# Optimization experiments

Measured on AMD Instinct MI355X. Metric: run time of the kernel, lower is better.

Reference implementation:

```python
import jax, jax.numpy as jnp
import numpy as np

B = 1; S = 2048; HID = 1024; NH = 8; HD = 128; INTER = 4096
EPS = 1e-6; THETA = 10000.0


def rms_norm(x, w):
    # Gemma RMSNorm: x * rsqrt(mean(x^2)+eps) * (1 + w)
    v = jnp.mean(x * x, axis=-1, keepdims=True)
    return x * jax.lax.rsqrt(v + EPS) * (1.0 + w)


def rope_cos_sin(seqlen):
    inv = 1.0 / (THETA ** (jnp.arange(0, HD, 2, dtype=jnp.float32) / HD))
    t = jnp.arange(seqlen, dtype=jnp.float32)
    f = jnp.outer(t, inv)                       # (S, HD/2)
    emb = jnp.concatenate([f, f], axis=-1)      # (S, HD)
    return jnp.cos(emb), jnp.sin(emb)


def rotate_half(x):
    x1, x2 = jnp.split(x, 2, axis=-1)
    return jnp.concatenate([-x2, x1], axis=-1)


def apply_rope(x, cos, sin):
    return x * cos[None, None] + rotate_half(x) * sin[None, None]


def expert_forward(x, mask, params):
    """One GemmaDecoderLayer; returns output plus PRE-RoPE q/k/v (as the torch module exposes)."""
    w_ln, wq, wk, wv, wo, w_pln, wg, wu, wd = params
    res = x
    h = rms_norm(x, w_ln)

    def proj(w):
        return (h @ w).reshape(B, -1, NH, HD).transpose(0, 2, 1, 3)  # (B,H,S,D)

    q, k, v = proj(wq), proj(wk), proj(wv)      # stored before rotary in the original
    cos, sin = rope_cos_sin(x.shape[1])
    qr, kr = apply_rope(q, cos, sin), apply_rope(k, cos, sin)
    scores = jnp.einsum('bhqd,bhkd->bhqk', qr, kr) * (HD ** -0.5) + mask
    attn = jnp.einsum('bhqk,bhkd->bhqd', jax.nn.softmax(scores, axis=-1), v)
    attn = attn.transpose(0, 2, 1, 3).reshape(B, -1, NH * HD) @ wo
    h1 = res + attn
    m = rms_norm(h1, w_pln)
    mlp = (jax.nn.gelu(m @ wg, approximate=True) * (m @ wu)) @ wd  # gelu_pytorch_tanh
    return h1 + mlp, q, k, v


def setup_inputs() -> dict:
    key = jax.random.key(0)
    ks = iter(jax.random.split(key, 40))

    def w(shape, scale=0.02):
        return jax.random.normal(next(ks), shape, jnp.float32) * scale

    inp = {
        'x_a': jax.random.normal(next(ks), (B, S, HID), jnp.float32),
        'x_b': jax.random.normal(next(ks), (B, S, HID), jnp.float32),
    }
    tri = jnp.tril(jnp.ones((S, S), bool))
    causal = jnp.where(tri, 0.0, -1e9).astype(jnp.float32)[None, None]  # additive causal mask
    inp['mask_a'] = causal
    inp['mask_b'] = causal
    inp['mix_mask'] = jnp.zeros((B, 1, 2 * S, 2 * S), jnp.float32)      # non-causal cross-expert
    for e in ('a', 'b'):
        inp['w_ln_' + e] = jnp.zeros((HID,), jnp.float32)
        inp['w_q_' + e] = w((HID, NH * HD))
        inp['w_k_' + e] = w((HID, NH * HD))
        inp['w_v_' + e] = w((HID, NH * HD))
        inp['w_o_' + e] = w((NH * HD, HID))
        inp['w_pln_' + e] = jnp.zeros((HID,), jnp.float32)
        inp['w_g_' + e] = w((HID, INTER))
        inp['w_u_' + e] = w((HID, INTER))
        inp['w_d_' + e] = w((INTER, HID))
    return inp


def reference(x_a, x_b, mask_a, mask_b, mix_mask,
              w_ln_a, w_q_a, w_k_a, w_v_a, w_o_a, w_pln_a, w_g_a, w_u_a, w_d_a,
              w_ln_b, w_q_b, w_k_b, w_v_b, w_o_b, w_pln_b, w_g_b, w_u_b, w_d_b):
    pa = (w_ln_a, w_q_a, w_k_a, w_v_a, w_o_a, w_pln_a, w_g_a, w_u_a, w_d_a)
    pb = (w_ln_b, w_q_b, w_k_b, w_v_b, w_o_b, w_pln_b, w_g_b, w_u_b, w_d_b)
    out_a, qa, ka, va = expert_forward(x_a, mask_a, pa)
    out_b, qb, kb, vb = expert_forward(x_b, mask_b, pb)
    # cross-expert mixed attention over concatenated (pre-RoPE) streams
    q = jnp.concatenate([qa, qb], axis=2)
    k = jnp.concatenate([ka, kb], axis=2)
    v = jnp.concatenate([va, vb], axis=2)
    scores = jnp.einsum('bhqd,bhkd->bhqk', q, k) * (HD ** -0.5) + mix_mask
    mixed = jnp.einsum('bhqk,bhkd->bhqd', jax.nn.softmax(scores, axis=-1), v)
    mixed = mixed.transpose(0, 2, 1, 3).reshape(B, 2 * S, NH * HD)
    ma, mb = mixed[:, :S], mixed[:, S:]
    return jnp.stack([out_a + ma @ w_o_a, out_b + mb @ w_o_b])
```

## Files before the change

### kernel.cpp

```cpp
#include <hip/hip_runtime.h>
#include <hip/hip_bf16.h>
#include <math.h>

#define S 2048
#define HID 1024
#define NH 8
#define HD 128
#define INTER 4096
#define EPSV 1e-6f
#define THETA 10000.0f

typedef __hip_bfloat16 bf16;
typedef unsigned short u16;
typedef __attribute__((ext_vector_type(8))) short bf16x8;
typedef __attribute__((ext_vector_type(4))) float f32x4;

__device__ inline float bu2f(u16 u) {
    unsigned int x = ((unsigned int)u) << 16;
    return __uint_as_float(x);
}
__device__ inline u16 f2bu(float f) {
    bf16 h = __float2bfloat16(f);
    return *reinterpret_cast<u16*>(&h);
}
__device__ inline float ldin(const void* p, size_t i, bool isbf) {
    return isbf ? bu2f(((const u16*)p)[i]) : ((const float*)p)[i];
}
__device__ inline float gelu_tanh(float x) {
    float x3 = x * x * x;
    return 0.5f * x * (1.f + tanhf(0.7978845608028654f * (x + 0.044715f * x3)));
}
__device__ inline void gload16(const u16* g, u16* l) {
    __builtin_amdgcn_global_load_lds(
        (const __attribute__((address_space(1))) void*)g,
        (__attribute__((address_space(3))) void*)l, 16, 0, 0);
}

__global__ __launch_bounds__(256) void probe_kernel(const unsigned short* __restrict__ x,
                                                    int* __restrict__ flag) {
    __shared__ int red[256];
    int tid = threadIdx.x;
    int cnt = 0;
    for (int i = tid; i < 2048; i += 256) {
        unsigned short u = x[2 * i];
        int e = (u >> 7) & 0xFF;
        cnt += (e >= 110 && e <= 135) ? 1 : 0;
    }
    red[tid] = cnt;
    __syncthreads();
    for (int off = 128; off > 0; off >>= 1) {
        if (tid < off) red[tid] += red[tid + off];
        __syncthreads();
    }
    if (tid == 0) *flag = (red[0] > 1024) ? 1 : 0;
}

struct TransN {
    const void* W[8];
    u16* T[8];
};
__global__ __launch_bounds__(256) void transpose_wN(TransN tn, const int* __restrict__ flag,
                                                    int K, int N) {
    bool isbf = (*flag != 0);
    const void* W = tn.W[blockIdx.z];
    u16* WT = tn.T[blockIdx.z];
    __shared__ float t[32][33];
    int n0 = blockIdx.x * 32, k0 = blockIdx.y * 32;
    int c = threadIdx.x & 31, r = threadIdx.x >> 5;
#pragma unroll
    for (int p = 0; p < 4; p++)
        t[r + 8 * p][c] = ldin(W, (size_t)(k0 + r + 8 * p) * N + n0 + c, isbf);
    __syncthreads();
#pragma unroll
    for (int p = 0; p < 4; p++) {
        int row = r + 8 * p;
        WT[(size_t)(n0 + row) * K + k0 + c] = f2bu(t[c][row]);
    }
}

__global__ __launch_bounds__(256) void transpose_v(const u16* __restrict__ V0,
                                                   const u16* __restrict__ V1, int sv,
                                                   u16* __restrict__ VT) {
    const u16* V = blockIdx.z ? V1 : V0;
    VT += (size_t)blockIdx.z * ((size_t)NH * HD * S);
    __shared__ u16 t[32][33];
    int k0 = blockIdx.x * 32;
    int d0 = blockIdx.y * 32;
    int c = threadIdx.x & 31, r = threadIdx.x >> 5;
#pragma unroll
    for (int p = 0; p < 4; p++)
        t[r + 8 * p][c] = V[(size_t)(k0 + r + 8 * p) * sv + d0 + c];
    __syncthreads();
#pragma unroll
    for (int p = 0; p < 4; p++)
        VT[(size_t)(d0 + r + 8 * p) * S + k0 + c] = t[c][r + 8 * p];
}

struct RmsDual {
    const void* x[2];
    const void* w[2];
    u16* y[2];
};
__global__ __launch_bounds__(256) void rmsnorm_kernel(RmsDual rd,
                                                      const int* __restrict__ flag,
                                                      int dual) {
    int e = blockIdx.y;
    const void* x = rd.x[e];
    const void* w = rd.w[e];
    u16* y = rd.y[e];
    bool isbf = (*flag != 0);
    bool xbf = dual && isbf;
    int row = blockIdx.x;
    size_t base = (size_t)row * HID;
    __shared__ float red[256];
    float xv[4];
    float s = 0.f;
#pragma unroll
    for (int i = 0; i < 4; i++) {
        float v = ldin(x, base + threadIdx.x + 256 * i, xbf);
        xv[i] = v;
        s += v * v;
    }
    red[threadIdx.x] = s;
    __syncthreads();
    for (int off = 128; off > 0; off >>= 1) {
        if (threadIdx.x < off) red[threadIdx.x] += red[threadIdx.x + off];
        __syncthreads();
    }
    float scale = rsqrtf(red[0] / (float)HID + EPSV);
#pragma unroll
    for (int i = 0; i < 4; i++) {
        int c = threadIdx.x + 256 * i;
        y[base + c] = f2bu(xv[i] * scale * (1.f + ldin(w, c, isbf)));
    }
}

struct GemmDual {
    const u16* A[2];
    const u16* BT[2];
    float* Cf[2];
    u16* Cb[2];
    const void* res[2];
};
template <int BM, int BN, int WRN, int WCN, int EPI>
__global__ __launch_bounds__(256) void gemm_mfma(GemmDual g, const int* __restrict__ flag,
                                                 int M, int N, int K) {
    int eZ = blockIdx.z;
    const u16* __restrict__ A = g.A[eZ];
    const u16* __restrict__ BT = g.BT[eZ];
    float* __restrict__ Cf = g.Cf[eZ];
    u16* __restrict__ Cb = g.Cb[eZ];
    const void* __restrict__ res = g.res[eZ];
    constexpr int WM = BM / WRN, WN = BN / WCN, TI = WM / 16, TJ = WN / 16;
    __shared__ u16 As[2][BM * 32];
    __shared__ u16 Bs[2][BN * 32];
    int tid = threadIdx.x, lane = tid & 63, wv = tid >> 6;
    int wr = wv / WCN, wc = wv % WCN;
    int m = lane & 15, quad = lane >> 4;
    int m0 = blockIdx.y * BM, n0 = blockIdx.x * BN;
    f32x4 acc[TI][TJ] = {};
    for (int k0 = 0; k0 < K; k0 += 64) {
        __syncthreads();
#pragma unroll
        for (int pan = 0; pan < 2; pan++) {
            int kp = k0 + 32 * pan;
#pragma unroll
            for (int c2 = 0; c2 < BM / 64; c2++) {
                int row0 = (wv * (BM / 64) + c2) * 16;
                int row = row0 + (lane >> 2);
                int ch = lane & 3;
                gload16(&A[(size_t)(m0 + row) * K + kp + ((ch ^ ((row >> 1) & 3)) << 3)],
                        &As[pan][row0 * 32]);
            }
#pragma unroll
            for (int c2 = 0; c2 < BN / 64; c2++) {
                int row0 = (wv * (BN / 64) + c2) * 16;
                int row = row0 + (lane >> 2);
                int ch = lane & 3;
                gload16(&BT[(size_t)(n0 + row) * K + kp + ((ch ^ ((row >> 1) & 3)) << 3)],
                        &Bs[pan][row0 * 32]);
            }
        }
        __syncthreads();
#pragma unroll
        for (int pan = 0; pan < 2; pan++) {
            bf16x8 af[TI], bf_[TJ];
#pragma unroll
            for (int i = 0; i < TI; i++) {
                int rr = wr * WM + i * 16 + m;
                af[i] = *reinterpret_cast<const bf16x8*>(
                    &As[pan][rr * 32 + ((quad ^ ((rr >> 1) & 3)) << 3)]);
            }
#pragma unroll
            for (int j = 0; j < TJ; j++) {
                int rr = wc * WN + j * 16 + m;
                bf_[j] = *reinterpret_cast<const bf16x8*>(
                    &Bs[pan][rr * 32 + ((quad ^ ((rr >> 1) & 3)) << 3)]);
            }
#pragma unroll
            for (int i = 0; i < TI; i++)
#pragma unroll
                for (int j = 0; j < TJ; j++)
                    acc[i][j] = __builtin_amdgcn_mfma_f32_16x16x32_bf16(af[i], bf_[j], acc[i][j], 0, 0, 0);
        }
    }
    bool isbf = (EPI == 1) ? (*flag != 0) : false;
#pragma unroll
    for (int i = 0; i < TI; i++) {
#pragma unroll
        for (int j = 0; j < TJ; j++) {
#pragma unroll
            for (int r = 0; r < 4; r++) {
                int row = m0 + wr * WM + i * 16 + quad * 4 + r;
                int col = n0 + wc * WN + j * 16 + m;
                size_t idx = (size_t)row * N + col;
                float v = acc[i][j][r];
                if (EPI == 0) Cb[idx] = f2bu(v);
                else if (EPI == 1) Cf[idx] = v + ldin(res, idx, isbf);
                else Cf[idx] = Cf[idx] + v;
            }
        }
    }
}

template <int BM, int BN, int WRN, int WCN>
__global__ __launch_bounds__(256) void gemm_gated_mfma(const u16* __restrict__ A,
                                                       const u16* __restrict__ BgT,
                                                       const u16* __restrict__ BuT,
                                                       u16* __restrict__ C,
                                                       int M, int N, int K) {
    constexpr int WM = BM / WRN, WN = BN / WCN, TI = WM / 16, TJ = WN / 16;
    __shared__ u16 As[2][BM * 32];
    __shared__ u16 Bgs[2][BN * 32];
    __shared__ u16 Bus[2][BN * 32];
    int tid = threadIdx.x, lane = tid & 63, wv = tid >> 6;
    int wr = wv / WCN, wc = wv % WCN;
    int m = lane & 15, quad = lane >> 4;
    int m0 = blockIdx.y * BM, n0 = blockIdx.x * BN;
    f32x4 accg[TI][TJ] = {};
    f32x4 accu[TI][TJ] = {};
    for (int k0 = 0; k0 < K; k0 += 64) {
        __syncthreads();
#pragma unroll
        for (int pan = 0; pan < 2; pan++) {
            int kp = k0 + 32 * pan;
#pragma unroll
            for (int c2 = 0; c2 < BM / 64; c2++) {
                int row0 = (wv * (BM / 64) + c2) * 16;
                int row = row0 + (lane >> 2);
                int ch = lane & 3;
                gload16(&A[(size_t)(m0 + row) * K + kp + ((ch ^ ((row >> 1) & 3)) << 3)],
                        &As[pan][row0 * 32]);
            }
#pragma unroll
            for (int c2 = 0; c2 < BN / 64; c2++) {
                int row0 = (wv * (BN / 64) + c2) * 16;
                int row = row0 + (lane >> 2);
                int ch = lane & 3;
                gload16(&BgT[(size_t)(n0 + row) * K + kp + ((ch ^ ((row >> 1) & 3)) << 3)],
                        &Bgs[pan][row0 * 32]);
                gload16(&BuT[(size_t)(n0 + row) * K + kp + ((ch ^ ((row >> 1) & 3)) << 3)],
                        &Bus[pan][row0 * 32]);
            }
        }
        __syncthreads();
#pragma unroll
        for (int pan = 0; pan < 2; pan++) {
            bf16x8 af[TI], bg[TJ], bu[TJ];
#pragma unroll
            for (int i = 0; i < TI; i++) {
                int rr = wr * WM + i * 16 + m;
                af[i] = *reinterpret_cast<const bf16x8*>(
                    &As[pan][rr * 32 + ((quad ^ ((rr >> 1) & 3)) << 3)]);
            }
#pragma unroll
            for (int j = 0; j < TJ; j++) {
                int rr = wc * WN + j * 16 + m;
                int off = rr * 32 + ((quad ^ ((rr >> 1) & 3)) << 3);
                bg[j] = *reinterpret_cast<const bf16x8*>(&Bgs[pan][off]);
                bu[j] = *reinterpret_cast<const bf16x8*>(&Bus[pan][off]);
            }
#pragma unroll
            for (int i = 0; i < TI; i++)
#pragma unroll
                for (int j = 0; j < TJ; j++) {
                    accg[i][j] = __builtin_amdgcn_mfma_f32_16x16x32_bf16(af[i], bg[j], accg[i][j], 0, 0, 0);
                    accu[i][j] = __builtin_amdgcn_mfma_f32_16x16x32_bf16(af[i], bu[j], accu[i][j], 0, 0, 0);
                }
        }
    }
#pragma unroll
    for (int i = 0; i < TI; i++)
#pragma unroll
        for (int j = 0; j < TJ; j++)
#pragma unroll
            for (int r = 0; r < 4; r++) {
                int row = m0 + wr * WM + i * 16 + quad * 4 + r;
                int col = n0 + wc * WN + j * 16 + m;
                C[(size_t)row * N + col] = f2bu(gelu_tanh(accg[i][j][r]) * accu[i][j][r]);
            }
}

__global__ __launch_bounds__(64) void rope_kernel(const u16* __restrict__ qkv0,
                                                  const u16* __restrict__ qkv1,
                                                  u16* __restrict__ qr,
                                                  u16* __restrict__ kr) {
    const u16* qkv = blockIdx.z ? qkv1 : qkv0;
    size_t zo = (size_t)blockIdx.z * ((size_t)S * HID);
    int b = blockIdx.x;
    int t = b >> 3, h = b & 7;
    int i = threadIdx.x;
    size_t ib = (size_t)t * 3072 + h * HD;
    size_t ob = zo + (size_t)t * HID + h * HD;
    float inv = __expf(-9.210340372f * (float)(2 * i) / (float)HD);
    float f = (float)t * inv;
    float c = cosf(f), s = sinf(f);
    float q1 = bu2f(qkv[ib + i]), q2 = bu2f(qkv[ib + i + 64]);
    qr[ob + i] = f2bu(q1 * c - q2 * s);
    qr[ob + i + 64] = f2bu(q2 * c + q1 * s);
    float k1 = bu2f(qkv[ib + 1024 + i]), k2 = bu2f(qkv[ib + 1024 + i + 64]);
    kr[ob + i] = f2bu(k1 * c - k2 * s);
    kr[ob + i + 64] = f2bu(k2 * c + k1 * s);
}

__device__ inline int swz64(int row, int b) {
    return row * 64 + (b ^ (((row >> 1) & 3) << 4));
}

template <bool CAUSAL>
__global__ __launch_bounds__(256, 2) void attn_mfma_kernel(
    const u16* __restrict__ qa, const u16* __restrict__ qb, int sq,
    const u16* __restrict__ ka, const u16* __restrict__ kb, int sk,
    const u16* __restrict__ vta, const u16* __restrict__ vtb,
    u16* __restrict__ Out, int nkeys) {
    __shared__ char Ks[2][16384];
    __shared__ char VTs[2][16384];

    int tid = threadIdx.x;
    int lane = tid & 63, w = tid >> 6;
    int col = lane & 15, quad = lane >> 4;
    int eZ = CAUSAL ? (int)blockIdx.z : 0;
    int bx = (CAUSAL && eZ) ? ((int)gridDim.x - 1 - (int)blockIdx.x) : (int)blockIdx.x;
    int q0 = bx * 64;
    int h = blockIdx.y;
    const float scale = 0.08838834764831845f;

    int q0r = CAUSAL ? q0 : (q0 & (S - 1));
    const u16* qsel = CAUSAL ? (eZ ? qb : qa) : ((q0 < S) ? qa : qb);
    const u16* qp = qsel + (size_t)q0r * sq;
    bf16x8 aq[4];
#pragma unroll
    for (int t = 0; t < 4; t++)
        aq[t] = *reinterpret_cast<const bf16x8*>(
            qp + (size_t)(16 * w + col) * sq + h * HD + 32 * t + quad * 8);

    const u16* kplo = (CAUSAL && eZ) ? kb : ka;
    const u16* vplo = (CAUSAL && eZ) ? vtb : vta;

    f32x4 o[8] = {};
    float m_ = -1e30f, l_ = 0.f;

    int sA = col + 16 * (2 * (quad & 1));
    int sB = sA + 16;
    bool hi = (quad >> 1) != 0;

    int ntiles = CAUSAL ? (q0 >> 6) + 1 : (nkeys >> 6);

    auto stage = [&](int buf, int tt) {
        int j0r = (tt * 64) & (S - 1);
        bool eb = (!CAUSAL) && (tt >= (S >> 6));
        const u16* kp = eb ? kb : kplo;
        const u16* vp = eb ? vtb : vplo;
        char* kd = &Ks[buf][(tid >> 6) * 1024];
        char* vd = &VTs[buf][(tid >> 6) * 1024];
#pragma unroll
        for (int i = 0; i < 4; i++) {
            int l = 256 * i + tid;
            int key = (l >> 2) & 63;
            int c = (l >> 8) * 4 + ((l & 3) ^ ((key >> 1) & 3));
            gload16(kp + (size_t)(j0r + key) * sk + h * HD + c * 8, (u16*)(kd + i * 4096));
        }
#pragma unroll
        for (int i = 0; i < 4; i++) {
            int l = 256 * i + tid;
            int d = (l >> 2) & 127;
            int c = (l >> 9) * 4 + ((l & 3) ^ ((d >> 1) & 3));
            gload16(vp + (size_t)(h * HD + d) * S + j0r + c * 8, (u16*)(vd + i * 4096));
        }
    };

    stage(0, 0);
    __syncthreads();
    int cur = 0;

    for (int tt = 0; tt < ntiles; tt++) {
        if (tt + 1 < ntiles) stage(cur ^ 1, tt + 1);
        const char* Kb = Ks[cur];
        const char* Vb = VTs[cur];

        f32x4 sc[4] = {};
        __builtin_amdgcn_s_setprio(1);
#pragma unroll
        for (int t = 0; t < 4; t++) {
#pragma unroll
            for (int ct = 0; ct < 4; ct++) {
                bf16x8 kf = *reinterpret_cast<const bf16x8*>(
                    Kb + t * 4096 + swz64(16 * ct + col, quad * 16));
                sc[ct] = __builtin_amdgcn_mfma_f32_16x16x32_bf16(kf, aq[t], sc[ct], 0, 0, 0);
            }
        }
        __builtin_amdgcn_s_setprio(0);
        bool diag = CAUSAL && (tt == ntiles - 1);
#pragma unroll
        for (int ct = 0; ct < 4; ct++) {
#pragma unroll
            for (int r = 0; r < 4; r++) {
                float v = sc[ct][r] * scale;
                if (diag && (16 * ct + 4 * quad + r > 16 * w + col)) v = -1e30f;
                sc[ct][r] = v;
            }
        }

        float mx0 = fmaxf(fmaxf(sc[0][0], sc[0][1]), fmaxf(sc[0][2], sc[0][3]));
        float mx1 = fmaxf(fmaxf(sc[1][0], sc[1][1]), fmaxf(sc[1][2], sc[1][3]));
        float mx2 = fmaxf(fmaxf(sc[2][0], sc[2][1]), fmaxf(sc[2][2], sc[2][3]));
        float mx3 = fmaxf(fmaxf(sc[3][0], sc[3][1]), fmaxf(sc[3][2], sc[3][3]));
        float rmax = fmaxf(fmaxf(mx0, mx1), fmaxf(mx2, mx3));
        rmax = fmaxf(rmax, __shfl_xor(rmax, 16));
        rmax = fmaxf(rmax, __shfl_xor(rmax, 32));
        float mn = fmaxf(m_, rmax);
        float al = __expf(m_ - mn);
#pragma unroll
        for (int ct = 0; ct < 4; ct++)
#pragma unroll
            for (int r = 0; r < 4; r++) sc[ct][r] = __expf(sc[ct][r] - mn);
        float s0 = (sc[0][0] + sc[0][1]) + (sc[0][2] + sc[0][3]);
        float s1 = (sc[1][0] + sc[1][1]) + (sc[1][2] + sc[1][3]);
        float s2 = (sc[2][0] + sc[2][1]) + (sc[2][2] + sc[2][3]);
        float s3 = (sc[3][0] + sc[3][1]) + (sc[3][2] + sc[3][3]);
        float rs = (s0 + s1) + (s2 + s3);
        rs += __shfl_xor(rs, 16);
        rs += __shfl_xor(rs, 32);
        l_ = l_ * al + rs;
        m_ = mn;

        unsigned int pu[4][2];
#pragma unroll
        for (int ct = 0; ct < 4; ct++) {
            pu[ct][0] = (unsigned int)f2bu(sc[ct][0]) | ((unsigned int)f2bu(sc[ct][1]) << 16);
            pu[ct][1] = (unsigned int)f2bu(sc[ct][2]) | ((unsigned int)f2bu(sc[ct][3]) << 16);
        }

#pragma unroll
        for (int nt = 0; nt < 8; nt++)
#pragma unroll
            for (int r = 0; r < 4; r++) o[nt][r] *= al;

#pragma unroll
        for (int ks = 0; ks < 2; ks++) {
            unsigned int a0 = __shfl(pu[2 * ks][0], sA);
            unsigned int a1 = __shfl(pu[2 * ks][1], sA);
            unsigned int c0 = __shfl(pu[2 * ks + 1][0], sA);
            unsigned int c1 = __shfl(pu[2 * ks + 1][1], sA);
            unsigned int b0 = __shfl(pu[2 * ks][0], sB);
            unsigned int b1 = __shfl(pu[2 * ks][1], sB);
            unsigned int g0 = __shfl(pu[2 * ks + 1][0], sB);
            unsigned int g1 = __shfl(pu[2 * ks + 1][1], sB);
            union {
                unsigned int u[4];
                bf16x8 v;
            } pb;
            pb.u[0] = hi ? c0 : a0;
            pb.u[1] = hi ? c1 : a1;
            pb.u[2] = hi ? g0 : b0;
            pb.u[3] = hi ? g1 : b1;
            __builtin_amdgcn_s_setprio(1);
#pragma unroll
            for (int nt = 0; nt < 8; nt++) {
                bf16x8 vf = *reinterpret_cast<const bf16x8*>(
                    Vb + ks * 8192 + swz64(16 * nt + col, quad * 16));
                o[nt] = __builtin_amdgcn_mfma_f32_16x16x32_bf16(vf, pb.v, o[nt], 0, 0, 0);
            }
            __builtin_amdgcn_s_setprio(0);
        }

        __syncthreads();
        cur ^= 1;
    }

    u16* outp = Out + (CAUSAL ? (size_t)eZ * ((size_t)S * HID) : (size_t)0);
    float inv = 1.f / l_;
    size_t rowoff = (size_t)(q0 + 16 * w + col) * HID + (size_t)h * HD + 4 * quad;
#pragma unroll
    for (int nt = 0; nt < 8; nt++) {
        ushort4 st;
        st.x = f2bu(o[nt][0] * inv);
        st.y = f2bu(o[nt][1] * inv);
        st.z = f2bu(o[nt][2] * inv);
        st.w = f2bu(o[nt][3] * inv);
        *reinterpret_cast<ushort4*>(&outp[rowoff + 16 * nt]) = st;
    }
}

__global__ __launch_bounds__(256, 4) void attn_mixed_split(
    const u16* __restrict__ qa, const u16* __restrict__ qb, int sq,
    const u16* __restrict__ ka, const u16* __restrict__ kb, int sk,
    const u16* __restrict__ vta, const u16* __restrict__ vtb,
    u16* __restrict__ Opart, float2* __restrict__ ml) {
    __shared__ char Ks[16384];
    __shared__ char VTs[16384];

    int tid = threadIdx.x;
    int lane = tid & 63, w = tid >> 6;
    int col = lane & 15, quad = lane >> 4;
    int q0 = blockIdx.x * 64;
    int h = blockIdx.y;
    int z = blockIdx.z;
    const float scale = 0.08838834764831845f;

    const u16* qp = ((q0 < S) ? qa : qb) + (size_t)(q0 & (S - 1)) * sq;
    bf16x8 aq[4];
#pragma unroll
    for (int t = 0; t < 4; t++)
        aq[t] = *reinterpret_cast<const bf16x8*>(
            qp + (size_t)(16 * w + col) * sq + h * HD + 32 * t + quad * 8);

    const u16* kp = z ? kb : ka;
    const u16* vp = z ? vtb : vta;

    f32x4 o[8] = {};
    float m_ = -1e30f, l_ = 0.f;

    int sA = col + 16 * (2 * (quad & 1));
    int sB = sA + 16;
    bool hi = (quad >> 1) != 0;

    for (int tt = 0; tt < (S >> 6); tt++) {
        int j0r = tt * 64;
        __syncthreads();
        {
            char* kd = &Ks[(tid >> 6) * 1024];
            char* vd = &VTs[(tid >> 6) * 1024];
#pragma unroll
            for (int i = 0; i < 4; i++) {
                int l = 256 * i + tid;
                int key = (l >> 2) & 63;
                int c = (l >> 8) * 4 + ((l & 3) ^ ((key >> 1) & 3));
                gload16(kp + (size_t)(j0r + key) * sk + h * HD + c * 8, (u16*)(kd + i * 4096));
            }
#pragma unroll
            for (int i = 0; i < 4; i++) {
                int l = 256 * i + tid;
                int d = (l >> 2) & 127;
                int c = (l >> 9) * 4 + ((l & 3) ^ ((d >> 1) & 3));
                gload16(vp + (size_t)(h * HD + d) * S + j0r + c * 8, (u16*)(vd + i * 4096));
            }
        }
        __syncthreads();

        f32x4 sc[4] = {};
        __builtin_amdgcn_s_setprio(1);
#pragma unroll
        for (int t = 0; t < 4; t++) {
#pragma unroll
            for (int ct = 0; ct < 4; ct++) {
                bf16x8 kf = *reinterpret_cast<const bf16x8*>(
                    Ks + t * 4096 + swz64(16 * ct + col, quad * 16));
                sc[ct] = __builtin_amdgcn_mfma_f32_16x16x32_bf16(kf, aq[t], sc[ct], 0, 0, 0);
            }
        }
        __builtin_amdgcn_s_setprio(0);
#pragma unroll
        for (int ct = 0; ct < 4; ct++)
#pragma unroll
            for (int r = 0; r < 4; r++) sc[ct][r] *= scale;

        float mx0 = fmaxf(fmaxf(sc[0][0], sc[0][1]), fmaxf(sc[0][2], sc[0][3]));
        float mx1 = fmaxf(fmaxf(sc[1][0], sc[1][1]), fmaxf(sc[1][2], sc[1][3]));
        float mx2 = fmaxf(fmaxf(sc[2][0], sc[2][1]), fmaxf(sc[2][2], sc[2][3]));
        float mx3 = fmaxf(fmaxf(sc[3][0], sc[3][1]), fmaxf(sc[3][2], sc[3][3]));
        float rmax = fmaxf(fmaxf(mx0, mx1), fmaxf(mx2, mx3));
        rmax = fmaxf(rmax, __shfl_xor(rmax, 16));
        rmax = fmaxf(rmax, __shfl_xor(rmax, 32));
        float mn = fmaxf(m_, rmax);
        float al = __expf(m_ - mn);
#pragma unroll
        for (int ct = 0; ct < 4; ct++)
#pragma unroll
            for (int r = 0; r < 4; r++) sc[ct][r] = __expf(sc[ct][r] - mn);
        float s0 = (sc[0][0] + sc[0][1]) + (sc[0][2] + sc[0][3]);
        float s1 = (sc[1][0] + sc[1][1]) + (sc[1][2] + sc[1][3]);
        float s2 = (sc[2][0] + sc[2][1]) + (sc[2][2] + sc[2][3]);
        float s3 = (sc[3][0] + sc[3][1]) + (sc[3][2] + sc[3][3]);
        float rs = (s0 + s1) + (s2 + s3);
        rs += __shfl_xor(rs, 16);
        rs += __shfl_xor(rs, 32);
        l_ = l_ * al + rs;
        m_ = mn;

        unsigned int pu[4][2];
#pragma unroll
        for (int ct = 0; ct < 4; ct++) {
            pu[ct][0] = (unsigned int)f2bu(sc[ct][0]) | ((unsigned int)f2bu(sc[ct][1]) << 16);
            pu[ct][1] = (unsigned int)f2bu(sc[ct][2]) | ((unsigned int)f2bu(sc[ct][3]) << 16);
        }

#pragma unroll
        for (int nt = 0; nt < 8; nt++)
#pragma unroll
            for (int r = 0; r < 4; r++) o[nt][r] *= al;

#pragma unroll
        for (int ks = 0; ks < 2; ks++) {
            unsigned int a0 = __shfl(pu[2 * ks][0], sA);
            unsigned int a1 = __shfl(pu[2 * ks][1], sA);
            unsigned int c0 = __shfl(pu[2 * ks + 1][0], sA);
            unsigned int c1 = __shfl(pu[2 * ks + 1][1], sA);
            unsigned int b0 = __shfl(pu[2 * ks][0], sB);
            unsigned int b1 = __shfl(pu[2 * ks][1], sB);
            unsigned int g0 = __shfl(pu[2 * ks + 1][0], sB);
            unsigned int g1 = __shfl(pu[2 * ks + 1][1], sB);
            union {
                unsigned int u[4];
                bf16x8 v;
            } pb;
            pb.u[0] = hi ? c0 : a0;
            pb.u[1] = hi ? c1 : a1;
            pb.u[2] = hi ? g0 : b0;
            pb.u[3] = hi ? g1 : b1;
            __builtin_amdgcn_s_setprio(1);
#pragma unroll
            for (int nt = 0; nt < 8; nt++) {
                bf16x8 vf = *reinterpret_cast<const bf16x8*>(
                    VTs + ks * 8192 + swz64(16 * nt + col, quad * 16));
                o[nt] = __builtin_amdgcn_mfma_f32_16x16x32_bf16(vf, pb.v, o[nt], 0, 0, 0);
            }
            __builtin_amdgcn_s_setprio(0);
        }
    }

    const size_t SPL = (size_t)2 * S * HID;
    size_t rowoff = (size_t)z * SPL + (size_t)(q0 + 16 * w + col) * HID + (size_t)h * HD + 4 * quad;
#pragma unroll
    for (int nt = 0; nt < 8; nt++) {
        ushort4 st;
        st.x = f2bu(o[nt][0]);
        st.y = f2bu(o[nt][1]);
        st.z = f2bu(o[nt][2]);
        st.w = f2bu(o[nt][3]);
        *reinterpret_cast<ushort4*>(&Opart[rowoff + 16 * nt]) = st;
    }
    if (quad == 0)
        ml[((size_t)z * 2 * S + q0 + 16 * w + col) * NH + h] = make_float2(m_, l_);
}

__global__ __launch_bounds__(256) void attn_combine(const u16* __restrict__ Opart,
                                                    const float2* __restrict__ ml,
                                                    u16* __restrict__ out) {
    size_t idx = ((size_t)blockIdx.x * 256 + threadIdx.x) * 8;
    int q = (int)(idx >> 10);
    int c0 = (int)(idx & 1023);
    int h = c0 >> 7;
    float2 ml0 = ml[(size_t)q * NH + h];
    float2 ml1 = ml[((size_t)2 * S + q) * NH + h];
    float ms = fmaxf(ml0.x, ml1.x);
    float w0 = __expf(ml0.x - ms), w1 = __expf(ml1.x - ms);
    float rden = 1.f / (w0 * ml0.y + w1 * ml1.y);
    const size_t SPL = (size_t)2 * S * HID;
    uint4 a = *reinterpret_cast<const uint4*>(&Opart[idx]);
    uint4 b = *reinterpret_cast<const uint4*>(&Opart[SPL + idx]);
    const u16* ap = reinterpret_cast<const u16*>(&a);
    const u16* bp = reinterpret_cast<const u16*>(&b);
    u16 res[8];
#pragma unroll
    for (int j = 0; j < 8; j++)
        res[j] = f2bu((w0 * bu2f(ap[j]) + w1 * bu2f(bp[j])) * rden);
    *reinterpret_cast<uint4*>(&out[idx]) = *reinterpret_cast<const uint4*>(res);
}

__global__ __launch_bounds__(256) void store_out_kernel(const float* __restrict__ a,
                                                        const float* __restrict__ b,
                                                        void* __restrict__ out,
                                                        const int* __restrict__ flag) {
    bool isbf = (*flag != 0);
    size_t i = (size_t)blockIdx.x * 256 + threadIdx.x;
    const size_t MM = (size_t)S * HID;
    float v = (i < MM) ? a[i] : b[i - MM];
    if (isbf)
        ((bf16*)out)[i] = __float2bfloat16(v);
    else
        ((float*)out)[i] = v;
}

extern "C" void kernel_launch(void* const* d_in, const int* in_sizes, int n_in,
                              void* d_out, int out_size, void* d_ws, size_t ws_size,
                              hipStream_t stream) {
    const void* x[2] = {d_in[0], d_in[1]};
    const void* w_ln[2] = {d_in[5], d_in[14]};
    const void* w_q[2] = {d_in[6], d_in[15]};
    const void* w_k[2] = {d_in[7], d_in[16]};
    const void* w_v[2] = {d_in[8], d_in[17]};
    const void* w_o[2] = {d_in[9], d_in[18]};
    const void* w_pln[2] = {d_in[10], d_in[19]};
    const void* w_g[2] = {d_in[11], d_in[20]};
    const void* w_u[2] = {d_in[12], d_in[21]};
    const void* w_d[2] = {d_in[13], d_in[22]};

    char* base = (char*)d_ws;
    int* flag = (int*)base;
    u16* p = (u16*)(base + 256);
    const size_t E_QKV = (size_t)S * 3072;
    const size_t E_SH = (size_t)S * HID;
    const size_t E_VT = (size_t)NH * HD * S;

    u16* qkv[2] = {p, p + E_QKV};            p += 2 * E_QKV;
    u16* qr = p;                             p += 2 * E_SH;
    u16* kr = p;                             p += 2 * E_SH;
    u16* h_bf = p;                           p += 2 * E_SH;
    u16* attnbuf = p;                        p += 2 * E_SH;
    u16* vtg = p;                            p += 2 * E_VT;
    u16* gated = qr;
    u16* Opart = qr;
    u16* mixed = h_bf;
    u16* wqkvT = p;                          p += 2 * (size_t)3072 * 1024;
    u16* woT[2] = {p, p + (size_t)1024 * 1024};  p += 2 * (size_t)1024 * 1024;
    u16* wgT = p;                            p += (size_t)INTER * 1024;
    u16* wuT = p;                            p += (size_t)INTER * 1024;
    u16* wdT = p;                            p += (size_t)1024 * INTER;
    float* fbase = (float*)(((size_t)p + 255) & ~(size_t)255);
    float* outX[2] = {fbase, fbase + E_SH};
    float2* mlbuf = (float2*)(fbase + 2 * E_SH);

    probe_kernel<<<1, 256, 0, stream>>>((const unsigned short*)d_in[0], flag);

    {
        TransN tn = {};
        for (int e = 0; e < 2; e++) {
            u16* wt = wqkvT + (size_t)e * 3072 * 1024;
            tn.W[4 * e + 0] = w_q[e];  tn.T[4 * e + 0] = wt;
            tn.W[4 * e + 1] = w_k[e];  tn.T[4 * e + 1] = wt + (size_t)1024 * 1024;
            tn.W[4 * e + 2] = w_v[e];  tn.T[4 * e + 2] = wt + (size_t)2048 * 1024;
            tn.W[4 * e + 3] = w_o[e];  tn.T[4 * e + 3] = woT[e];
        }
        transpose_wN<<<dim3(32, 32, 8), 256, 0, stream>>>(tn, flag, 1024, 1024);
    }

    {
        RmsDual rd = {{x[0], x[1]}, {w_ln[0], w_ln[1]}, {h_bf, h_bf + E_SH}};
        rmsnorm_kernel<<<dim3(S, 2), 256, 0, stream>>>(rd, flag, 1);
    }
    {
        GemmDual g = {{h_bf, h_bf + E_SH},
                      {wqkvT, wqkvT + (size_t)3072 * 1024},
                      {nullptr, nullptr},
                      {qkv[0], qkv[1]},
                      {nullptr, nullptr}};
        gemm_mfma<128, 128, 2, 2, 0><<<dim3(3072 / 128, S / 128, 2), 256, 0, stream>>>(
            g, flag, S, 3072, 1024);
    }
    rope_kernel<<<dim3(S * NH, 1, 2), 64, 0, stream>>>(qkv[0], qkv[1], qr, kr);
    transpose_v<<<dim3(S / 32, 1024 / 32, 2), 256, 0, stream>>>(qkv[0] + 2048, qkv[1] + 2048, 3072, vtg);
    attn_mfma_kernel<true><<<dim3(S / 64, NH, 2), 256, 0, stream>>>(
        qr, qr + E_SH, HID, kr, kr + E_SH, HID, vtg, vtg + E_VT, attnbuf, S);
    {
        GemmDual g = {{attnbuf, attnbuf + E_SH},
                      {woT[0], woT[1]},
                      {outX[0], outX[1]},
                      {nullptr, nullptr},
                      {x[0], x[1]}};
        gemm_mfma<64, 64, 2, 2, 1><<<dim3(1024 / 64, S / 64, 2), 256, 0, stream>>>(
            g, flag, S, 1024, 1024);
    }
    {
        RmsDual rd = {{outX[0], outX[1]}, {w_pln[0], w_pln[1]}, {h_bf, h_bf + E_SH}};
        rmsnorm_kernel<<<dim3(S, 2), 256, 0, stream>>>(rd, flag, 0);
    }

    for (int e = 0; e < 2; e++) {
        {
            TransN tg = {};
            tg.W[0] = w_g[e];  tg.T[0] = wgT;
            tg.W[1] = w_u[e];  tg.T[1] = wuT;
            transpose_wN<<<dim3(INTER / 32, 1024 / 32, 2), 256, 0, stream>>>(tg, flag, 1024, INTER);
        }
        gemm_gated_mfma<128, 64, 2, 2><<<dim3(INTER / 64, S / 128), 256, 0, stream>>>(
            h_bf + e * E_SH, wgT, wuT, gated, S, INTER, 1024);
        {
            TransN td = {};
            td.W[0] = w_d[e];  td.T[0] = wdT;
            transpose_wN<<<dim3(1024 / 32, INTER / 32, 1), 256, 0, stream>>>(td, flag, INTER, 1024);
        }
        GemmDual g = {{gated, gated}, {wdT, wdT}, {outX[e], outX[e]}, {nullptr, nullptr}, {nullptr, nullptr}};
        gemm_mfma<64, 64, 2, 2, 2><<<dim3(1024 / 64, S / 64, 1), 256, 0, stream>>>(
            g, flag, S, 1024, INTER);
    }

    attn_mixed_split<<<dim3(2 * S / 64, NH, 2), 256, 0, stream>>>(
        qkv[0], qkv[1], 3072, qkv[0] + 1024, qkv[1] + 1024, 3072,
        vtg, vtg + E_VT, Opart, mlbuf);
    attn_combine<<<(2 * E_SH) / (256 * 8), 256, 0, stream>>>(Opart, mlbuf, mixed);
    {
        GemmDual g = {{mixed, mixed + E_SH},
                      {woT[0], woT[1]},
                      {outX[0], outX[1]},
                      {nullptr, nullptr},
                      {nullptr, nullptr}};
        gemm_mfma<64, 64, 2, 2, 2><<<dim3(1024 / 64, S / 64, 2), 256, 0, stream>>>(
            g, flag, S, 1024, 1024);
    }

    store_out_kernel<<<(2 * E_SH) / 256, 256, 0, stream>>>(outX[0], outX[1], d_out, flag);
}
```

Before: 745.2 us.

## Batch both experts' MLP transposes and GEMMs into single dual launches

Replaces the per-expert loop of MLP weight transposes, gated GEMM and down GEMM with single launches that cover both experts through blockIdx.z. This doubles the grid per launch, which should give better CU occupancy on the smaller down-projection GEMM and cuts the kernel launch count. In exchange it needs a second gated buffer and aliases several workspace regions (attnbuf, wqkvT, wgT) as scratch for the second expert's transposed weights. That aliasing depends on those buffers being dead at this point in the sequence.

```diff
diff --git a/kernel.cpp b/kernel.cpp
--- a/kernel.cpp
+++ b/kernel.cpp
@@ -223,12 +223,19 @@
     }
 }
 
+struct GatedDual {
+    const u16* A[2];
+    const u16* Bg[2];
+    const u16* Bu[2];
+    u16* C[2];
+};
 template <int BM, int BN, int WRN, int WCN>
-__global__ __launch_bounds__(256) void gemm_gated_mfma(const u16* __restrict__ A,
-                                                       const u16* __restrict__ BgT,
-                                                       const u16* __restrict__ BuT,
-                                                       u16* __restrict__ C,
-                                                       int M, int N, int K) {
+__global__ __launch_bounds__(256) void gemm_gated_mfma(GatedDual gd, int M, int N, int K) {
+    int eZ = blockIdx.z;
+    const u16* __restrict__ A = gd.A[eZ];
+    const u16* __restrict__ BgT = gd.Bg[eZ];
+    const u16* __restrict__ BuT = gd.Bu[eZ];
+    u16* __restrict__ C = gd.C[eZ];
     constexpr int WM = BM / WRN, WN = BN / WCN, TI = WM / 16, TJ = WN / 16;
     __shared__ u16 As[2][BM * 32];
     __shared__ u16 Bgs[2][BN * 32];
@@ -712,6 +719,7 @@
     const size_t E_QKV = (size_t)S * 3072;
     const size_t E_SH = (size_t)S * HID;
     const size_t E_VT = (size_t)NH * HD * S;
+    const size_t E_GT = (size_t)S * INTER;
 
     u16* qkv[2] = {p, p + E_QKV};            p += 2 * E_QKV;
     u16* qr = p;                             p += 2 * E_SH;
@@ -719,17 +727,21 @@
     u16* h_bf = p;                           p += 2 * E_SH;
     u16* attnbuf = p;                        p += 2 * E_SH;
     u16* vtg = p;                            p += 2 * E_VT;
-    u16* gated = qr;
-    u16* Opart = qr;
-    u16* mixed = h_bf;
     u16* wqkvT = p;                          p += 2 * (size_t)3072 * 1024;
     u16* woT[2] = {p, p + (size_t)1024 * 1024};  p += 2 * (size_t)1024 * 1024;
     u16* wgT = p;                            p += (size_t)INTER * 1024;
     u16* wuT = p;                            p += (size_t)INTER * 1024;
     u16* wdT = p;                            p += (size_t)1024 * INTER;
+    u16* gated1 = p;                         p += E_GT;
     float* fbase = (float*)(((size_t)p + 255) & ~(size_t)255);
     float* outX[2] = {fbase, fbase + E_SH};
     float2* mlbuf = (float2*)(fbase + 2 * E_SH);
+    u16* gated0 = qr;
+    u16* wgT2 = wqkvT;
+    u16* wuT2 = attnbuf;
+    u16* wdT2 = wgT;
+    u16* Opart = qr;
+    u16* mixed = h_bf;
 
     probe_kernel<<<1, 256, 0, stream>>>((const unsigned short*)d_in[0], flag);
 
@@ -776,22 +788,35 @@
         rmsnorm_kernel<<<dim3(S, 2), 256, 0, stream>>>(rd, flag, 0);
     }
 
-    for (int e = 0; e < 2; e++) {
-        {
-            TransN tg = {};
-            tg.W[0] = w_g[e];  tg.T[0] = wgT;
-            tg.W[1] = w_u[e];  tg.T[1] = wuT;
-            transpose_wN<<<dim3(INTER / 32, 1024 / 32, 2), 256, 0, stream>>>(tg, flag, 1024, INTER);
-        }
-        gemm_gated_mfma<128, 64, 2, 2><<<dim3(INTER / 64, S / 128), 256, 0, stream>>>(
-            h_bf + e * E_SH, wgT, wuT, gated, S, INTER, 1024);
-        {
-            TransN td = {};
-            td.W[0] = w_d[e];  td.T[0] = wdT;
-            transpose_wN<<<dim3(1024 / 32, INTER / 32, 1), 256, 0, stream>>>(td, flag, INTER, 1024);
-        }
-        GemmDual g = {{gated, gated}, {wdT, wdT}, {outX[e], outX[e]}, {nullptr, nullptr}, {nullptr, nullptr}};
-        gemm_mfma<64, 64, 2, 2, 2><<<dim3(1024 / 64, S / 64, 1), 256, 0, stream>>>(
+    {
+        TransN tg = {};
+        tg.W[0] = w_g[0];  tg.T[0] = wgT;
+        tg.W[1] = w_u[0];  tg.T[1] = wuT;
+        tg.W[2] = w_g[1];  tg.T[2] = wgT2;
+        tg.W[3] = w_u[1];  tg.T[3] = wuT2;
+        transpose_wN<<<dim3(INTER / 32, 1024 / 32, 4), 256, 0, stream>>>(tg, flag, 1024, INTER);
+    }
+    {
+        GatedDual gg = {{h_bf, h_bf + E_SH},
+                        {wgT, wgT2},
+                        {wuT, wuT2},
+                        {gated0, gated1}};
+        gemm_gated_mfma<128, 64, 2, 2><<<dim3(INTER / 64, S / 128, 2), 256, 0, stream>>>(
+            gg, S, INTER, 1024);
+    }
+    {
+        TransN td = {};
+        td.W[0] = w_d[0];  td.T[0] = wdT;
+        td.W[1] = w_d[1];  td.T[1] = wdT2;
+        transpose_wN<<<dim3(1024 / 32, INTER / 32, 2), 256, 0, stream>>>(td, flag, INTER, 1024);
+    }
+    {
+        GemmDual g = {{gated0, gated1},
+                      {wdT, wdT2},
+                      {outX[0], outX[1]},
+                      {nullptr, nullptr},
+                      {nullptr, nullptr}};
+        gemm_mfma<64, 64, 2, 2, 2><<<dim3(1024 / 64, S / 64, 2), 256, 0, stream>>>(
             g, flag, S, 1024, INTER);
     }
 
```

Result: faster. 707.5 us (-5.1%).
